# Kernel tuning notes

Measured on AMD Instinct MI355X. Metric: run time of the kernel, lower is better.

## Reference

```python
import jax, jax.numpy as jnp
import numpy as np

NUM_CLASSES = 9
BASE_SMOOTHING = 0.1
UPWARD_BIAS = 0.2
BATCH = 4_000_000


def setup_inputs() -> dict:
    key = jax.random.key(0)
    k1, k2 = jax.random.split(key)
    logits = jax.random.normal(k1, (BATCH, NUM_CLASSES), dtype=jnp.float32)
    targets = jax.random.randint(k2, (BATCH,), 0, NUM_CLASSES, dtype=jnp.int32)
    return {"logits": logits, "targets": targets}


def _smooth_labels(targets, num_classes):
    # Closed form of the per-sample Python loop in the torch module:
    #   label[t] = 1 - bs - ub  (set, overwriting the base)
    #   label[k] = bs/C + ub * 0.5**(k - t)   for k > t (geometric halving,
    #              including the last class which keeps remaining*0.5)
    #   label[k] = bs/C                        for k < t
    # followed by row normalization.
    base = BASE_SMOOTHING / num_classes
    main = 1.0 - BASE_SMOOTHING - UPWARD_BIAS
    j = jnp.arange(num_classes)  # [C]
    d = j[None, :] - targets[:, None]  # [B, C], class index minus target
    upward = jnp.where(d > 0, UPWARD_BIAS * jnp.exp2(-d.astype(jnp.float32)), 0.0)
    labels = jnp.where(d == 0, main, base + upward)  # [B, C]
    return labels / labels.sum(axis=-1, keepdims=True)


def reference(logits, targets):
    smooth = _smooth_labels(targets, logits.shape[-1])  # [B, C]
    log_probs = jax.nn.log_softmax(logits, axis=-1)      # [B, C]
    loss = -(smooth * log_probs).sum(axis=-1)            # [B]
    return loss.mean()
```

## Files before the change

### kernel.cpp

```cpp
#include <hip/hip_runtime.h>
#include <math.h>

#define NUM_C 9
constexpr float W_BASE = 0.1f / 9.0f;
constexpr float W_MAIN = 0.7f;

constexpr int THREADS = 256;
constexpr int ROWS_PER_BLOCK = 1024;
constexpr int VECS_PER_BLOCK = ROWS_PER_BLOCK * NUM_C / 4;
constexpr int VECS_PER_WAVE = VECS_PER_BLOCK / 4;
constexpr int CALLS_PER_WAVE = VECS_PER_WAVE / 64;

__device__ __forceinline__ void async_copy16(const float4* g, float4* l) {
    __builtin_amdgcn_global_load_lds(
        (const __attribute__((address_space(1))) void*)g,
        (__attribute__((address_space(3))) void*)l,
        16 , 0 , 0 );
}

__global__ __launch_bounds__(THREADS, 4) void ccel_main(
    const float* __restrict__ logits,
    const int* __restrict__ targets,
    float* __restrict__ partials,
    int nRows, int nFullBlocks)
{
    __shared__ float4 lds4[VECS_PER_BLOCK];
    __shared__ float wave_sums[THREADS / 64];

    const int tid = threadIdx.x;
    const int wave = tid >> 6;
    const int lane = tid & 63;
    const long long vecBase = (long long)blockIdx.x * VECS_PER_BLOCK;
    const float4* gv = (const float4*)logits + vecBase;

    const int myRow = blockIdx.x * ROWS_PER_BLOCK + tid * 4;
    int4 t4 = {0, 0, 0, 0};
    if (myRow < nRows) t4 = ((const int4*)targets)[myRow >> 2];

    if (blockIdx.x < nFullBlocks) {
        const float4* src = gv + wave * VECS_PER_WAVE;
        float4* dst = lds4 + wave * VECS_PER_WAVE;
#pragma unroll
        for (int i = 0; i < CALLS_PER_WAVE; i++) {
            async_copy16(src + i * 64 + lane, dst + i * 64);
        }
    } else {
        const long long totalVecs = ((long long)nRows * NUM_C) / 4;
        for (int i = tid; i < VECS_PER_BLOCK; i += THREADS) {
            if (vecBase + i < totalVecs) lds4[i] = gv[i];
        }
    }
    __syncthreads();

    float acc = 0.0f;

    if (myRow < nRows) {
        const int tg[4] = {t4.x, t4.y, t4.z, t4.w};

        float x[36];
        float4* xv = (float4*)x;
#pragma unroll
        for (int i = 0; i < 9; i++) xv[i] = lds4[tid * 9 + i];

#pragma unroll
        for (int k = 0; k < 4; k++) {
            const float* xr = x + k * NUM_C;
            const int t = tg[k];

            float m = xr[0];
#pragma unroll
            for (int j = 1; j < NUM_C; j++) m = fmaxf(m, xr[j]);

            float sum = 0.0f, xt = 0.0f;
#pragma unroll
            for (int j = 0; j < NUM_C; j++) {
                sum += xr[j];
                xt = (t == j) ? xr[j] : xt;
            }

            float g = 0.0f, gt = 0.0f;
#pragma unroll
            for (int j = NUM_C - 1; j >= 1; j--) {
                g = 0.5f * (xr[j] + g);
                gt = (t == j - 1) ? g : gt;
            }

            float es = 0.0f;
#pragma unroll
            for (int j = 0; j < NUM_C; j++) es += __expf(xr[j] - m);
            const float lse = m + __logf(es);

            const float S = 0.98888889f - 0.2f * ldexpf(1.0f, t - 8);
            const float weighted = W_BASE * sum + (W_MAIN - W_BASE) * xt + 0.2f * gt;
            acc += lse - weighted * __builtin_amdgcn_rcpf(S);
        }
    }

#pragma unroll
    for (int off = 32; off > 0; off >>= 1)
        acc += __shfl_down(acc, off, 64);

    if (lane == 0) wave_sums[wave] = acc;
    __syncthreads();
    if (tid == 0) {
        float bsum = 0.0f;
#pragma unroll
        for (int w = 0; w < THREADS / 64; w++) bsum += wave_sums[w];
        partials[blockIdx.x] = bsum;
    }
}

__global__ __launch_bounds__(1024) void ccel_finish(
    const float* __restrict__ partials,
    int n,
    float* __restrict__ out,
    float invBatch)
{
    double acc = 0.0;
    for (int i = threadIdx.x; i < n; i += 1024)
        acc += (double)partials[i];

#pragma unroll
    for (int off = 32; off > 0; off >>= 1)
        acc += __shfl_down(acc, off, 64);

    __shared__ double wsum[16];
    if ((threadIdx.x & 63) == 0) wsum[threadIdx.x >> 6] = acc;
    __syncthreads();
    if (threadIdx.x == 0) {
        double total = 0.0;
#pragma unroll
        for (int w = 0; w < 16; w++) total += wsum[w];
        out[0] = (float)(total * (double)invBatch);
    }
}

extern "C" void kernel_launch(void* const* d_in, const int* in_sizes, int n_in,
                              void* d_out, int out_size, void* d_ws, size_t ws_size,
                              hipStream_t stream) {
    const float* logits = (const float*)d_in[0];
    const int* targets = (const int*)d_in[1];
    const int nRows = in_sizes[1];

    float* partials = (float*)d_ws;
    const int nBlocks = (nRows + ROWS_PER_BLOCK - 1) / ROWS_PER_BLOCK;
    const long long totalVecs = ((long long)nRows * NUM_C) / 4;
    const int nFullBlocks = (int)(totalVecs / VECS_PER_BLOCK);

    ccel_main<<<nBlocks, THREADS, 0, stream>>>(logits, targets, partials,
                                               nRows, nFullBlocks);
    ccel_finish<<<1, 1024, 0, stream>>>(partials, nBlocks, (float*)d_out,
                                        1.0f / (float)nRows);
}
```

Measured before the change: 212.5 us.

## Use persistent double-buffered async LDS staging for logits and targets

Replaces the one-block-per-chunk launch with a fixed grid of 512 persistent blocks. Each block loops over 1024-row chunks and prefetches the next chunk into a second LDS buffer while computing the current one. Targets are now also staged into LDS asynchronously, and waits use per-wave vmcnt/lgkmcnt counters instead of block barriers. The aim is to overlap global loads with compute and cut launch and tail overhead. In exchange, LDS per block doubles to about 80KB, occupancy hint drops to 2 blocks, and the partial-tail rows are handled by a separate path.

```diff
diff --git a/kernel.cpp b/kernel.cpp
--- a/kernel.cpp
+++ b/kernel.cpp
@@ -6,93 +6,132 @@
 constexpr float W_MAIN = 0.7f;
 
 constexpr int THREADS = 256;
-constexpr int ROWS_PER_BLOCK = 1024;
-constexpr int VECS_PER_BLOCK = ROWS_PER_BLOCK * NUM_C / 4;
-constexpr int VECS_PER_WAVE = VECS_PER_BLOCK / 4;
+constexpr int GRID = 512;
+constexpr int CHUNK_ROWS = 1024;
+constexpr int VECS_PER_CHUNK = CHUNK_ROWS * NUM_C / 4;
+constexpr int VECS_PER_WAVE  = VECS_PER_CHUNK / 4;
 constexpr int CALLS_PER_WAVE = VECS_PER_WAVE / 64;
+constexpr int TVECS_PER_CHUNK = CHUNK_ROWS / 4;
 
-__device__ __forceinline__ void async_copy16(const float4* g, float4* l) {
+__device__ __forceinline__ void async_copy16(const void* g, void* l) {
     __builtin_amdgcn_global_load_lds(
         (const __attribute__((address_space(1))) void*)g,
         (__attribute__((address_space(3))) void*)l,
         16 , 0 , 0 );
 }
 
-__global__ __launch_bounds__(THREADS, 4) void ccel_main(
+__device__ __forceinline__ void stage_chunk(
+    const float4* __restrict__ logv, const int4* __restrict__ tgtv,
+    float4* lbuf, int4* tbuf, int chunk, int wave, int lane)
+{
+    const float4* src = logv + (long long)chunk * VECS_PER_CHUNK + wave * VECS_PER_WAVE;
+    float4* dst = lbuf + wave * VECS_PER_WAVE;
+#pragma unroll
+    for (int i = 0; i < CALLS_PER_WAVE; i++)
+        async_copy16(src + i * 64 + lane, dst + i * 64);
+    async_copy16(tgtv + (long long)chunk * TVECS_PER_CHUNK + wave * 64 + lane,
+                 tbuf + wave * 64);
+}
+
+__device__ __forceinline__ float rows4_loss(const float* x, const int4& t4) {
+    const int tg[4] = {t4.x, t4.y, t4.z, t4.w};
+    float acc = 0.0f;
+#pragma unroll
+    for (int k = 0; k < 4; k++) {
+        const float* xr = x + k * NUM_C;
+        const int t = tg[k];
+
+        float m = xr[0];
+#pragma unroll
+        for (int j = 1; j < NUM_C; j++) m = fmaxf(m, xr[j]);
+
+        float sum = 0.0f, xt = 0.0f;
+#pragma unroll
+        for (int j = 0; j < NUM_C; j++) {
+            sum += xr[j];
+            xt = (t == j) ? xr[j] : xt;
+        }
+
+        float g = 0.0f, gt = 0.0f;
+#pragma unroll
+        for (int j = NUM_C - 1; j >= 1; j--) {
+            g = 0.5f * (xr[j] + g);
+            gt = (t == j - 1) ? g : gt;
+        }
+
+        float es = 0.0f;
+#pragma unroll
+        for (int j = 0; j < NUM_C; j++) es += __expf(xr[j] - m);
+        const float lse = m + __logf(es);
+
+        const float S = 0.98888889f - 0.2f * ldexpf(1.0f, t - 8);
+        const float weighted = W_BASE * sum + (W_MAIN - W_BASE) * xt + 0.2f * gt;
+        acc += lse - weighted * __builtin_amdgcn_rcpf(S);
+    }
+    return acc;
+}
+
+__global__ __launch_bounds__(THREADS, 2) void ccel_main(
     const float* __restrict__ logits,
     const int* __restrict__ targets,
     float* __restrict__ partials,
-    int nRows, int nFullBlocks)
+    int nRows)
 {
-    __shared__ float4 lds4[VECS_PER_BLOCK];
-    __shared__ float wave_sums[THREADS / 64];
+    __shared__ float4 lds4[2][VECS_PER_CHUNK];
+    __shared__ int4   tlds[2][TVECS_PER_CHUNK];
 
-    const int tid = threadIdx.x;
+    const int tid  = threadIdx.x;
     const int wave = tid >> 6;
     const int lane = tid & 63;
-    const long long vecBase = (long long)blockIdx.x * VECS_PER_BLOCK;
-    const float4* gv = (const float4*)logits + vecBase;
+    const int bid  = blockIdx.x;
 
-    const int myRow = blockIdx.x * ROWS_PER_BLOCK + tid * 4;
-    int4 t4 = {0, 0, 0, 0};
-    if (myRow < nRows) t4 = ((const int4*)targets)[myRow >> 2];
+    const float4* logv = (const float4*)logits;
+    const int4*   tgtv = (const int4*)targets;
 
-    if (blockIdx.x < nFullBlocks) {
-        const float4* src = gv + wave * VECS_PER_WAVE;
-        float4* dst = lds4 + wave * VECS_PER_WAVE;
-#pragma unroll
-        for (int i = 0; i < CALLS_PER_WAVE; i++) {
-            async_copy16(src + i * 64 + lane, dst + i * 64);
-        }
-    } else {
-        const long long totalVecs = ((long long)nRows * NUM_C) / 4;
-        for (int i = tid; i < VECS_PER_BLOCK; i += THREADS) {
-            if (vecBase + i < totalVecs) lds4[i] = gv[i];
-        }
-    }
-    __syncthreads();
+    const int nFull = nRows / CHUNK_ROWS;
 
     float acc = 0.0f;
 
-    if (myRow < nRows) {
-        const int tg[4] = {t4.x, t4.y, t4.z, t4.w};
+    if (bid < nFull)
+        stage_chunk(logv, tgtv, &lds4[0][0], &tlds[0][0], bid, wave, lane);
+
+    int cur = 0;
+    for (int c = bid; c < nFull; c += GRID) {
+        const int cn = c + GRID;
+        asm volatile("s_waitcnt lgkmcnt(0)" ::: "memory");
+        if (cn < nFull) {
+            stage_chunk(logv, tgtv, &lds4[cur ^ 1][0], &tlds[cur ^ 1][0],
+                        cn, wave, lane);
+            asm volatile("s_waitcnt vmcnt(10)" ::: "memory");
+        } else {
+            asm volatile("s_waitcnt vmcnt(0)" ::: "memory");
+        }
+        __builtin_amdgcn_sched_barrier(0);
 
         float x[36];
         float4* xv = (float4*)x;
 #pragma unroll
-        for (int i = 0; i < 9; i++) xv[i] = lds4[tid * 9 + i];
+        for (int i = 0; i < 9; i++) xv[i] = lds4[cur][tid * 9 + i];
+        const int4 t4 = tlds[cur][tid];
 
+        acc += rows4_loss(x, t4);
+
+        __builtin_amdgcn_sched_barrier(0);
+        cur ^= 1;
+    }
+
+    const int tailRows = nRows - nFull * CHUNK_ROWS;
+    if (tailRows > 0 && bid == (nFull % GRID)) {
+        const long long rowBase = (long long)nFull * CHUNK_ROWS;
+        const int myRow = tid * 4;
+        if (myRow + 4 <= tailRows) {
+            float x[36];
+            float4* xv = (float4*)x;
+            const float4* gp = logv + (rowBase * NUM_C) / 4 + tid * 9;
 #pragma unroll
-        for (int k = 0; k < 4; k++) {
-            const float* xr = x + k * NUM_C;
-            const int t = tg[k];
-
-            float m = xr[0];
-#pragma unroll
-            for (int j = 1; j < NUM_C; j++) m = fmaxf(m, xr[j]);
-
-            float sum = 0.0f, xt = 0.0f;
-#pragma unroll
-            for (int j = 0; j < NUM_C; j++) {
-                sum += xr[j];
-                xt = (t == j) ? xr[j] : xt;
-            }
-
-            float g = 0.0f, gt = 0.0f;
-#pragma unroll
-            for (int j = NUM_C - 1; j >= 1; j--) {
-                g = 0.5f * (xr[j] + g);
-                gt = (t == j - 1) ? g : gt;
-            }
-
-            float es = 0.0f;
-#pragma unroll
-            for (int j = 0; j < NUM_C; j++) es += __expf(xr[j] - m);
-            const float lse = m + __logf(es);
-
-            const float S = 0.98888889f - 0.2f * ldexpf(1.0f, t - 8);
-            const float weighted = W_BASE * sum + (W_MAIN - W_BASE) * xt + 0.2f * gt;
-            acc += lse - weighted * __builtin_amdgcn_rcpf(S);
+            for (int i = 0; i < 9; i++) xv[i] = gp[i];
+            const int4 t4 = tgtv[rowBase / 4 + tid];
+            acc += rows4_loss(x, t4);
         }
     }
 
@@ -100,13 +139,15 @@
     for (int off = 32; off > 0; off >>= 1)
         acc += __shfl_down(acc, off, 64);
 
-    if (lane == 0) wave_sums[wave] = acc;
+    __syncthreads();
+    float* wsum = (float*)&tlds[0][0];
+    if (lane == 0) wsum[wave] = acc;
     __syncthreads();
     if (tid == 0) {
         float bsum = 0.0f;
 #pragma unroll
-        for (int w = 0; w < THREADS / 64; w++) bsum += wave_sums[w];
-        partials[blockIdx.x] = bsum;
+        for (int w = 0; w < THREADS / 64; w++) bsum += wsum[w];
+        partials[bid] = bsum;
     }
 }
 
@@ -143,12 +184,8 @@
     const int nRows = in_sizes[1];
 
     float* partials = (float*)d_ws;
-    const int nBlocks = (nRows + ROWS_PER_BLOCK - 1) / ROWS_PER_BLOCK;
-    const long long totalVecs = ((long long)nRows * NUM_C) / 4;
-    const int nFullBlocks = (int)(totalVecs / VECS_PER_BLOCK);
 
-    ccel_main<<<nBlocks, THREADS, 0, stream>>>(logits, targets, partials,
-                                               nRows, nFullBlocks);
-    ccel_finish<<<1, 1024, 0, stream>>>(partials, nBlocks, (float*)d_out,
+    ccel_main<<<GRID, THREADS, 0, stream>>>(logits, targets, partials, nRows);
+    ccel_finish<<<1, 1024, 0, stream>>>(partials, GRID, (float*)d_out,
                                         1.0f / (float)nRows);
 }
```

Result: slower. 217.0 us (+2.1%).
